# Kernel optimization log

Measured on AMD Instinct MI355X. Metric: run time of the kernel, lower is better.

Reference implementation:

```python
import jax, jax.numpy as jnp
import numpy as np
import math

B, N, D, H = 8, 1024, 512, 8
DH = D // H  # 64
FF = 4 * D   # 2048
SQRT_2_OVER_PI = math.sqrt(2.0 / math.pi)
LN_EPS = 1e-12


def gelu_new(x):
    # tanh-approx GELU as in DenseGatedGeluDense.gelu_new
    return 0.5 * x * (1.0 + jnp.tanh(SQRT_2_OVER_PI * (x + 0.044715 * x ** 3)))


def layer_norm(x, scale, bias):
    m = jnp.mean(x, axis=-1, keepdims=True)
    v = jnp.mean((x - m) ** 2, axis=-1, keepdims=True)
    return (x - m) * jax.lax.rsqrt(v + LN_EPS) * scale + bias


def setup_inputs() -> dict:
    key = jax.random.key(0)
    ks = jax.random.split(key, 12)
    w = lambda k, shape: (jax.random.normal(k, shape, jnp.float32) * 0.02)
    return {
        "X": jax.random.normal(ks[0], (B, N, D), jnp.float32),
        "train_ind": jax.random.randint(ks[1], (B, N), 0, 2).astype(jnp.int32),
        "batch_ind": jax.random.randint(ks[2], (B, N), 0, 2).astype(jnp.int32),
        "Wq": w(ks[3], (D, D)), "bq": jnp.zeros((D,), jnp.float32),
        "Wk": w(ks[4], (D, D)), "bk": jnp.zeros((D,), jnp.float32),
        "Wv": w(ks[5], (D, D)), "bv": jnp.zeros((D,), jnp.float32),
        "Wmix": w(ks[6], (D, D)), "bmix": jnp.zeros((D,), jnp.float32),
        "ln0_s": jnp.ones((D,), jnp.float32), "ln0_b": jnp.zeros((D,), jnp.float32),
        "ln1_s": jnp.ones((D,), jnp.float32), "ln1_b": jnp.zeros((D,), jnp.float32),
        "wi0": w(ks[7], (D, FF)),
        "wi1": w(ks[8], (D, FF)),
        "wo": w(ks[9], (FF, D)),
    }


def reference(X, train_ind, batch_ind, Wq, bq, Wk, bk, Wv, bv, Wmix, bmix,
              ln0_s, ln0_b, ln1_s, ln1_b, wi0, wi1, wo):
    # --- MAB with self-attention (SAB: Y = X), pre-LayerNorm variant ---
    Xn = layer_norm(X, ln0_s, ln0_b)          # ln0 applied to query side only
    Q = Xn @ Wq + bq                           # (B, N, D)
    X_res = Q                                  # fc_res is None -> residual = Q
    K = X @ Wk + bk                            # K/V computed from raw Y (=X)
    V = X @ Wv + bv

    Qh = Q.reshape(B, N, H, DH)
    Kh = K.reshape(B, N, H, DH)
    Vh = V.reshape(B, N, H, DH)

    # scores scaled by sqrt(dim_KV) per att_score_norm == 'softmax'
    scores = jnp.einsum("bqhd,bkhd->bhqk", Qh, Kh) / math.sqrt(D)  # (B,H,N,N)

    # get_attention_mask: key j attendable iff j in train or batch set, or j == i
    allowed_key = (train_ind + batch_ind) != 0                     # (B, N)
    allow = allowed_key[:, None, :] | jnp.eye(N, dtype=bool)[None] # (B, N, N)
    scores = jnp.where(allow[:, None, :, :], scores, -jnp.inf)

    A = jax.nn.softmax(scores, axis=-1)
    O = jnp.einsum("bhqk,bkhd->bqhd", A, Vh).reshape(B, N, D)

    Hc = O @ Wmix + bmix                       # fc_mix_heads
    Hc = X_res + Hc                            # residual (pre-LN branch)

    # GEGLU rFF block (DenseGatedGeluDense), pre-LN
    x1 = layer_norm(Hc, ln1_s, ln1_b)
    ff = (gelu_new(x1 @ wi0) * (x1 @ wi1)) @ wo
    return Hc + ff
```

## Files before the change

### kernel.cpp

```cpp
#include <hip/hip_runtime.h>
#include <hip/hip_bf16.h>
#include <math.h>

#define DEV __device__ __forceinline__

using bf16x8 = __attribute__((ext_vector_type(8))) short;
using f32x4  = __attribute__((ext_vector_type(4))) float;

static constexpr int Bb = 8, Nn = 1024, Dd = 512, Hh = 8, DHd = 64, FFd = 2048;
static constexpr int Mrows = Bb * Nn;

DEV short f2bf(float f) {
  union { float f; unsigned u; } v; v.f = f;
  unsigned r = v.u + 0x7fffu + ((v.u >> 16) & 1u);
  return (short)(r >> 16);
}
DEV float bf2f(short s) {
  union { unsigned u; float f; } v; v.u = ((unsigned)(unsigned short)s) << 16;
  return v.f;
}
DEV float fexp2(float x) { return __builtin_amdgcn_exp2f(x); }

DEV f32x4 mfma16(bf16x8 a, bf16x8 b, f32x4 c) {
  return __builtin_amdgcn_mfma_f32_16x16x32_bf16(a, b, c, 0, 0, 0);
}

DEV size_t swz(int r, int k, int ld) {
  return (size_t)(r >> 6) * 64 * ld + (size_t)(k >> 3) * 512
       + (size_t)((r & 63) * 8 + (k & 7));
}

DEV void gload16(const void* g, void* l) {
  __builtin_amdgcn_global_load_lds(
      (const __attribute__((address_space(1))) void*)g,
      (__attribute__((address_space(3))) void*)l, 16, 0, 0);
}

DEV float gelu_fast(float g) {
  float u2l = 2.30220822f * (g + 0.044715f * g * g * g);
  return g / (1.0f + fexp2(-u2l));
}

DEV void xcd_tile2(int wg, int gx, int gy, int& trow, int& tcol) {
  int xcd = wg & 7, idx = wg >> 3;
  int XC = (gx >= 16) ? 2 : 1, XR = 8 / XC;
  int lcx = gx / XC, lcy = gy / XR;
  trow = (xcd / XC) * lcy + idx / lcx;
  tcol = (xcd % XC) * lcx + idx % lcx;
}

struct PreArgs {
  const float* src[7]; short* dst[7];
  const int* train; const int* batch; char* allowC;
  const float* X; const float* sc; const float* bi;
  short* xn; short* xraw;
};
__global__ __launch_bounds__(256)
void k_preprocess(PreArgs a) {
  __shared__ float tile[32][33];
  int id = blockIdx.x;
  if (id < 4096) {
    int j, rem;
    if (id < 1024)      { j = id >> 8;                 rem = id & 255; }
    else if (id < 3072) { j = 4 + ((id - 1024) >> 10); rem = (id - 1024) & 1023; }
    else                { j = 6;                       rem = id - 3072; }
    int K = (j == 6) ? 2048 : 512;
    int N = (j == 4 || j == 5) ? 2048 : 512;
    const float* W = a.src[j];
    short* WT = a.dst[j];
    int gx = N >> 5;
    int nb = (rem % gx) * 32, kb = (rem / gx) * 32;
    int tx = threadIdx.x & 31, ty = threadIdx.x >> 5;
    #pragma unroll
    for (int i = ty; i < 32; i += 8)
      tile[i][tx] = W[(size_t)(kb + i) * N + nb + tx];
    __syncthreads();
    #pragma unroll
    for (int i = ty; i < 32; i += 8)
      WT[swz(nb + i, kb + tx, K)] = f2bf(tile[tx][i]);
  } else if (id < 4128) {
    int i = (id - 4096) * 256 + threadIdx.x;
    a.allowC[i] = ((a.train[i] | a.batch[i]) != 0) ? 1 : 0;
  } else {
    int w = threadIdx.x >> 6, lane = threadIdx.x & 63;
    int row = (id - 4128) * 4 + w;
    const float* x = a.X + (size_t)row * Dd + lane * 8;
    f32x4 va = *(const f32x4*)x;
    f32x4 vb = *(const f32x4*)(x + 4);
    float p = va[0] + va[1] + va[2] + va[3] + vb[0] + vb[1] + vb[2] + vb[3];
    #pragma unroll
    for (int off = 1; off < 64; off <<= 1) p += __shfl_xor(p, off);
    float mean = p * (1.0f / Dd);
    float d[8];
    #pragma unroll
    for (int j = 0; j < 4; j++) { d[j] = va[j] - mean; d[4 + j] = vb[j] - mean; }
    float q = 0.0f;
    #pragma unroll
    for (int j = 0; j < 8; j++) q += d[j] * d[j];
    #pragma unroll
    for (int off = 1; off < 64; off <<= 1) q += __shfl_xor(q, off);
    float rs = rsqrtf(q * (1.0f / Dd) + 1e-12f);
    int c0 = lane * 8;
    f32x4 s0 = *(const f32x4*)(a.sc + c0), s1 = *(const f32x4*)(a.sc + c0 + 4);
    f32x4 b0 = *(const f32x4*)(a.bi + c0), b1 = *(const f32x4*)(a.bi + c0 + 4);
    bf16x8 o;
    #pragma unroll
    for (int j = 0; j < 4; j++) {
      o[j]     = f2bf(d[j] * rs * s0[j] + b0[j]);
      o[4 + j] = f2bf(d[4 + j] * rs * s1[j] + b1[j]);
    }
    *(bf16x8*)(a.xn + swz(row, c0, Dd)) = o;
    bf16x8 rv;
    #pragma unroll
    for (int j = 0; j < 4; j++) { rv[j] = f2bf(va[j]); rv[4 + j] = f2bf(vb[j]); }
    *(bf16x8*)(a.xraw + swz(row, c0, Dd)) = rv;
  }
}

__global__ __launch_bounds__(256)
void k_layernorm1(const float* __restrict__ X, const float* __restrict__ sc,
                  const float* __restrict__ bi, short* __restrict__ out) {
  int w = threadIdx.x >> 6, lane = threadIdx.x & 63;
  int row = blockIdx.x * 4 + w;
  const float* x = X + (size_t)row * Dd + lane * 8;
  f32x4 a = *(const f32x4*)x;
  f32x4 b = *(const f32x4*)(x + 4);
  float p = a[0] + a[1] + a[2] + a[3] + b[0] + b[1] + b[2] + b[3];
  #pragma unroll
  for (int off = 1; off < 64; off <<= 1) p += __shfl_xor(p, off);
  float mean = p * (1.0f / Dd);
  float d[8];
  #pragma unroll
  for (int j = 0; j < 4; j++) { d[j] = a[j] - mean; d[4 + j] = b[j] - mean; }
  float q = 0.0f;
  #pragma unroll
  for (int j = 0; j < 8; j++) q += d[j] * d[j];
  #pragma unroll
  for (int off = 1; off < 64; off <<= 1) q += __shfl_xor(q, off);
  float rs = rsqrtf(q * (1.0f / Dd) + 1e-12f);
  int c0 = lane * 8;
  f32x4 s0 = *(const f32x4*)(sc + c0), s1 = *(const f32x4*)(sc + c0 + 4);
  f32x4 b0 = *(const f32x4*)(bi + c0), b1 = *(const f32x4*)(bi + c0 + 4);
  bf16x8 o;
  #pragma unroll
  for (int j = 0; j < 4; j++) {
    o[j]     = f2bf(d[j] * rs * s0[j] + b0[j]);
    o[4 + j] = f2bf(d[4 + j] * rs * s1[j] + b1[j]);
  }
  *(bf16x8*)(out + swz(row, c0, Dd)) = o;
}

template<int BN, int BK, int BIASM, int RESM, bool WF, bool WB, int EPI>
__global__ __launch_bounds__(256, 4)
void k_gemm128(const short* __restrict__ A, const short* __restrict__ BT,
               const float* __restrict__ bias, const float* __restrict__ resF,
               const short* __restrict__ resB, const short* __restrict__ gpre,
               float* __restrict__ outF, short* __restrict__ outB,
               int M, int N, int K) {
  constexpr int FN = BN / 32;
  __shared__ short lA[2][128 * BK];
  __shared__ short lB[2][BN * BK];
  int tid = threadIdx.x, w = tid >> 6, lane = tid & 63;
  int lr = lane & 15, lg = lane >> 4;
  int wr = w >> 1, wc = w & 1;
  int trow, tcol;
  xcd_tile2(blockIdx.y * gridDim.x + blockIdx.x, gridDim.x, gridDim.y, trow, tcol);
  int row0 = trow * 128, col0 = tcol * BN;
  f32x4 acc[4][FN] = {};

  auto stage = [&](int buf, int k0) {
    #pragma unroll
    for (int i = 0; i < BK / 16; i++) {
      int c = i * 4 + w;
      gload16(A + swz(row0 + (c & 1) * 64 + lane, k0 + (c >> 1) * 8, K),
              &lA[buf][c * 512]);
    }
    #pragma unroll
    for (int i = 0; i < (BN * BK) / 2048; i++) {
      int c = i * 4 + w;
      if (BN == 128)
        gload16(BT + swz(col0 + (c & 1) * 64 + lane, k0 + (c >> 1) * 8, K),
                &lB[buf][c * 512]);
      else
        gload16(BT + swz(col0 + lane, k0 + c * 8, K), &lB[buf][c * 512]);
    }
  };

  stage(0, 0);
  __syncthreads();
  int nt = K / BK, buf = 0;
  for (int t = 0; t < nt; t++) {
    if (t + 1 < nt) stage(buf ^ 1, (t + 1) * BK);
    #pragma unroll
    for (int kk = 0; kk < BK / 32; kk++) {
      bf16x8 af[4];
      #pragma unroll
      for (int m = 0; m < 4; m++)
        af[m] = *(const bf16x8*)&lA[buf][(kk * 4 + lg) * 1024 + (wr * 64 + m * 16 + lr) * 8];
      #pragma unroll
      for (int n = 0; n < FN; n++) {
        bf16x8 bfr = *(const bf16x8*)&lB[buf][(kk * 4 + lg) * (BN * 8)
                                              + (wc * (BN / 2) + n * 16 + lr) * 8];
        #pragma unroll
        for (int m = 0; m < 4; m++)
          acc[m][n] = mfma16(af[m], bfr, acc[m][n]);
      }
    }
    __syncthreads();
    buf ^= 1;
  }

  #pragma unroll
  for (int n = 0; n < FN; n++) {
    int col = col0 + wc * (BN / 2) + n * 16 + lr;
    float bv = (BIASM == 1) ? bias[col] : 0.0f;
    #pragma unroll
    for (int m = 0; m < 4; m++) {
      #pragma unroll
      for (int r = 0; r < 4; r++) {
        int rowg = row0 + wr * 64 + m * 16 + lg * 4 + r;
        float vv = acc[m][n][r] + bv;
        if (BIASM == 2) vv += bias[rowg];
        if (RESM == 1) vv += resF[(size_t)rowg * N + col];
        if (RESM == 2) vv += bf2f(resB[swz(rowg, col, N)]);
        if (EPI == 1) vv = gelu_fast(vv);
        if (EPI == 2) vv *= bf2f(gpre[swz(rowg, col, N)]);
        if (WF) outF[(size_t)rowg * N + col] = vv;
        if (WB) outB[swz(rowg, col, N)] = f2bf(vv);
      }
    }
  }
}

__global__ __launch_bounds__(256, 4)
void k_qkv(const short* __restrict__ Xnbf, const short* __restrict__ Xbf,
           const short* __restrict__ WqT, const short* __restrict__ WkT,
           const short* __restrict__ WvT,
           const float* __restrict__ bq, const float* __restrict__ bk,
           const float* __restrict__ bv,
           short* __restrict__ Qbf, short* __restrict__ Kbf,
           short* __restrict__ VTg) {
  constexpr int BN = 64, BK = 64, FN = 2;
  constexpr int K = 512;
  __shared__ short lA[2][128 * BK];
  __shared__ short lB[2][BN * BK];
  int id = blockIdx.x;
  int which = id >> 9, sub = id & 511;
  const short *A, *BT; const float* bias; short* outB;
  int N, gx, gy; bool rowbias;
  if (which == 0)      { A = Xnbf; BT = WqT; bias = bq; outB = Qbf; N = 512;  gx = 8;   gy = 64; rowbias = false; }
  else if (which == 1) { A = Xbf;  BT = WkT; bias = bk; outB = Kbf; N = 512;  gx = 8;   gy = 64; rowbias = false; }
  else                 { A = WvT;  BT = Xbf; bias = bv; outB = VTg; N = 8192; gx = 128; gy = 4;  rowbias = true;  }
  int tid = threadIdx.x, w = tid >> 6, lane = tid & 63;
  int lr = lane & 15, lg = lane >> 4;
  int wr = w >> 1, wc = w & 1;
  int trow, tcol;
  xcd_tile2(sub, gx, gy, trow, tcol);
  int row0 = trow * 128, col0 = tcol * BN;
  f32x4 acc[4][FN] = {};

  auto stage = [&](int buf, int k0) {
    #pragma unroll
    for (int i = 0; i < BK / 16; i++) {
      int c = i * 4 + w;
      gload16(A + swz(row0 + (c & 1) * 64 + lane, k0 + (c >> 1) * 8, K),
              &lA[buf][c * 512]);
    }
    #pragma unroll
    for (int i = 0; i < (BN * BK) / 2048; i++) {
      int c = i * 4 + w;
      gload16(BT + swz(col0 + lane, k0 + c * 8, K), &lB[buf][c * 512]);
    }
  };

  stage(0, 0);
  __syncthreads();
  int nt = K / BK, buf = 0;
  for (int t = 0; t < nt; t++) {
    if (t + 1 < nt) stage(buf ^ 1, (t + 1) * BK);
    #pragma unroll
    for (int kk = 0; kk < BK / 32; kk++) {
      bf16x8 af[4];
      #pragma unroll
      for (int m = 0; m < 4; m++)
        af[m] = *(const bf16x8*)&lA[buf][(kk * 4 + lg) * 1024 + (wr * 64 + m * 16 + lr) * 8];
      #pragma unroll
      for (int n = 0; n < FN; n++) {
        bf16x8 bfr = *(const bf16x8*)&lB[buf][(kk * 4 + lg) * (BN * 8)
                                              + (wc * (BN / 2) + n * 16 + lr) * 8];
        #pragma unroll
        for (int m = 0; m < 4; m++)
          acc[m][n] = mfma16(af[m], bfr, acc[m][n]);
      }
    }
    __syncthreads();
    buf ^= 1;
  }

  #pragma unroll
  for (int n = 0; n < FN; n++) {
    int col = col0 + wc * (BN / 2) + n * 16 + lr;
    float bvc = rowbias ? 0.0f : bias[col];
    #pragma unroll
    for (int m = 0; m < 4; m++) {
      #pragma unroll
      for (int r = 0; r < 4; r++) {
        int rowg = row0 + wr * 64 + m * 16 + lg * 4 + r;
        float vv = acc[m][n][r] + bvc;
        if (rowbias) vv += bias[rowg];
        outB[swz(rowg, col, N)] = f2bf(vv);
      }
    }
  }
}

__global__ __launch_bounds__(256, 2)
void k_attention(const short* __restrict__ Qbf, const short* __restrict__ Kbf,
                 const short* __restrict__ VT, const char* __restrict__ allowC,
                 short* __restrict__ Obf) {
  __shared__ __align__(16) short Plds[4][32][72];
  __shared__ float maskF[Nn];
  int bid = blockIdx.x;
  int h = bid & 7, b = (bid >> 3) & 7, qt = bid >> 6;
  int tid = threadIdx.x, w = tid >> 6, lane = tid & 63, lr = lane & 15, lg = lane >> 4;
  int q0 = qt * 128 + w * 32;

  {
    const char* ac = allowC + b * Nn;
    #pragma unroll
    for (int j = 0; j < 4; j++) {
      int i = tid * 4 + j;
      maskF[i] = ac[i] ? 0.0f : -1e30f;
    }
  }
  __syncthreads();

  bf16x8 aq[2][2];
  #pragma unroll
  for (int qi = 0; qi < 2; qi++)
  #pragma unroll
  for (int j = 0; j < 2; j++)
    aq[qi][j] = *(const bf16x8*)(Qbf + swz(b * Nn + q0 + qi * 16 + lr,
                                           h * 64 + j * 32 + lg * 8, Dd));
  f32x4 acco[2][4] = {};
  float m_run[2][4], l_run[2][4];
  #pragma unroll
  for (int qi = 0; qi < 2; qi++)
  #pragma unroll
  for (int r = 0; r < 4; r++) { m_run[qi][r] = 0.0f; l_run[qi][r] = 0.0f; }
  const float scale2 = 0.06375871573f;

  auto loadK = [&](bf16x8 (&kf)[4][2], int kb) {
    #pragma unroll
    for (int sub = 0; sub < 4; sub++)
    #pragma unroll
    for (int j = 0; j < 2; j++)
      kf[sub][j] = *(const bf16x8*)(Kbf + swz(b * Nn + kb + sub * 16 + lr,
                                              h * 64 + j * 32 + lg * 8, Dd));
  };

  auto process = [&](bf16x8 (&kf)[4][2], int kb, bf16x8 (&kfn)[4][2], int kbn) {
    loadK(kfn, kbn);
    bf16x8 vb[2][4];
    #pragma unroll
    for (int ks = 0; ks < 2; ks++)
    #pragma unroll
    for (int t = 0; t < 4; t++)
      vb[ks][t] = *(const bf16x8*)(VT + swz(h * 64 + t * 16 + lr,
                                            b * Nn + kb + ks * 32 + lg * 8, Mrows));
    f32x4 accs[2][4] = {};
    #pragma unroll
    for (int sub = 0; sub < 4; sub++) {
      #pragma unroll
      for (int qi = 0; qi < 2; qi++) {
        accs[qi][sub] = mfma16(aq[qi][0], kf[sub][0], accs[qi][sub]);
        accs[qi][sub] = mfma16(aq[qi][1], kf[sub][1], accs[qi][sub]);
      }
    }
    float mk[4];
    #pragma unroll
    for (int sub = 0; sub < 4; sub++) mk[sub] = maskF[kb + sub * 16 + lr];
    float sv[2][4][4];
    #pragma unroll
    for (int qi = 0; qi < 2; qi++)
    #pragma unroll
    for (int sub = 0; sub < 4; sub++)
    #pragma unroll
    for (int r = 0; r < 4; r++)
      sv[qi][sub][r] = accs[qi][sub][r] * scale2 + mk[sub];
    if (kb == (q0 & ~63)) {
      #pragma unroll
      for (int qi = 0; qi < 2; qi++)
      #pragma unroll
      for (int sub = 0; sub < 4; sub++) {
        int key = kb + sub * 16 + lr;
        #pragma unroll
        for (int r = 0; r < 4; r++) {
          int qrow = q0 + qi * 16 + lg * 4 + r;
          if (key == qrow) sv[qi][sub][r] = accs[qi][sub][r] * scale2;
        }
      }
    }
    bool allok = true;
    float pmax[2][4];
    #pragma unroll
    for (int qi = 0; qi < 2; qi++)
    #pragma unroll
    for (int r = 0; r < 4; r++) {
      pmax[qi][r] = fmaxf(fmaxf(sv[qi][0][r], sv[qi][1][r]),
                          fmaxf(sv[qi][2][r], sv[qi][3][r]));
      allok = allok && (pmax[qi][r] <= m_run[qi][r] + 11.5416f);
    }
    if (!__all(allok)) {
      #pragma unroll
      for (int qi = 0; qi < 2; qi++)
      #pragma unroll
      for (int r = 0; r < 4; r++) {
        float m = pmax[qi][r];
        #pragma unroll
        for (int off = 1; off < 16; off <<= 1) m = fmaxf(m, __shfl_xor(m, off));
        float mtot = fmaxf(m_run[qi][r], m);
        float alpha = fexp2(m_run[qi][r] - mtot);
        l_run[qi][r] *= alpha;
        m_run[qi][r] = mtot;
        #pragma unroll
        for (int t = 0; t < 4; t++) acco[qi][t][r] *= alpha;
      }
    }
    #pragma unroll
    for (int qi = 0; qi < 2; qi++)
    #pragma unroll
    for (int sub = 0; sub < 4; sub++)
    #pragma unroll
    for (int r = 0; r < 4; r++) {
      float e = fexp2(sv[qi][sub][r] - m_run[qi][r]);
      l_run[qi][r] += e;
      Plds[w][qi * 16 + lg * 4 + r][sub * 16 + lr] = f2bf(e);
    }
    #pragma unroll
    for (int ks = 0; ks < 2; ks++) {
      bf16x8 pa0 = *(const bf16x8*)(&Plds[w][lr][ks * 32 + lg * 8]);
      bf16x8 pa1 = *(const bf16x8*)(&Plds[w][16 + lr][ks * 32 + lg * 8]);
      #pragma unroll
      for (int t = 0; t < 4; t++) {
        acco[0][t] = mfma16(pa0, vb[ks][t], acco[0][t]);
        acco[1][t] = mfma16(pa1, vb[ks][t], acco[1][t]);
      }
    }
  };

  bf16x8 kfA[4][2], kfB[4][2];
  loadK(kfA, 0);
  for (int kb = 0; kb < Nn; kb += 128) {
    int n1 = kb + 64;
    int n2 = (kb + 128 < Nn) ? (kb + 128) : 0;
    process(kfA, kb, kfB, n1);
    process(kfB, n1, kfA, n2);
  }

  #pragma unroll
  for (int qi = 0; qi < 2; qi++)
  #pragma unroll
  for (int r = 0; r < 4; r++) {
    float lsum = l_run[qi][r];
    #pragma unroll
    for (int off = 1; off < 16; off <<= 1) lsum += __shfl_xor(lsum, off);
    l_run[qi][r] = lsum;
  }
  #pragma unroll
  for (int qi = 0; qi < 2; qi++)
  #pragma unroll
  for (int t = 0; t < 4; t++)
  #pragma unroll
  for (int r = 0; r < 4; r++) {
    int q = b * Nn + q0 + qi * 16 + lg * 4 + r;
    Obf[swz(q, h * 64 + t * 16 + lr, Dd)] = f2bf(acco[qi][t][r] / l_run[qi][r]);
  }
}

extern "C" void kernel_launch(void* const* d_in, const int* in_sizes, int n_in,
                              void* d_out, int out_size, void* d_ws, size_t ws_size,
                              hipStream_t stream) {
  const float* X    = (const float*)d_in[0];
  const int*   train= (const int*)d_in[1];
  const int*   batch= (const int*)d_in[2];
  const float* Wq   = (const float*)d_in[3];
  const float* bq   = (const float*)d_in[4];
  const float* Wk   = (const float*)d_in[5];
  const float* bk   = (const float*)d_in[6];
  const float* Wv   = (const float*)d_in[7];
  const float* bv   = (const float*)d_in[8];
  const float* Wmix = (const float*)d_in[9];
  const float* bmix = (const float*)d_in[10];
  const float* ln0s = (const float*)d_in[11];
  const float* ln0b = (const float*)d_in[12];
  const float* ln1s = (const float*)d_in[13];
  const float* ln1b = (const float*)d_in[14];
  const float* wi0  = (const float*)d_in[15];
  const float* wi1  = (const float*)d_in[16];
  const float* wo   = (const float*)d_in[17];
  float* out = (float*)d_out;

  char* ws = (char*)d_ws;
  size_t off = 0;
  auto alloc = [&](size_t bytes) {
    off = (off + 255) & ~(size_t)255;
    void* p = ws + off; off += bytes; return p;
  };
  short* Xbf   = (short*)alloc((size_t)Mrows * Dd * 2);
  short* Xnbf  = (short*)alloc((size_t)Mrows * Dd * 2);
  short* Qbf   = (short*)alloc((size_t)Mrows * Dd * 2);
  short* Kbf   = (short*)alloc((size_t)Mrows * Dd * 2);
  short* VTg   = (short*)alloc((size_t)Dd * Mrows * 2);
  short* Obf   = (short*)alloc((size_t)Mrows * Dd * 2);
  short* x1bf  = (short*)alloc((size_t)Mrows * Dd * 2);
  short* Gbf   = (short*)alloc((size_t)Mrows * FFd * 2);
  short* FFbf  = (short*)alloc((size_t)Mrows * FFd * 2);
  short* WqT   = (short*)alloc((size_t)Dd * Dd * 2);
  short* WkT   = (short*)alloc((size_t)Dd * Dd * 2);
  short* WvT   = (short*)alloc((size_t)Dd * Dd * 2);
  short* WmixT = (short*)alloc((size_t)Dd * Dd * 2);
  short* wi0T  = (short*)alloc((size_t)FFd * Dd * 2);
  short* wi1T  = (short*)alloc((size_t)FFd * Dd * 2);
  short* woT   = (short*)alloc((size_t)Dd * FFd * 2);
  float* Hcf   = (float*)alloc((size_t)Mrows * Dd * 4);
  char*  allowC= (char*)alloc((size_t)Mrows);

  dim3 blk(256);
  PreArgs pa;
  pa.src[0] = Wq;   pa.dst[0] = WqT;
  pa.src[1] = Wk;   pa.dst[1] = WkT;
  pa.src[2] = Wv;   pa.dst[2] = WvT;
  pa.src[3] = Wmix; pa.dst[3] = WmixT;
  pa.src[4] = wi0;  pa.dst[4] = wi0T;
  pa.src[5] = wi1;  pa.dst[5] = wi1T;
  pa.src[6] = wo;   pa.dst[6] = woT;
  pa.train = train; pa.batch = batch; pa.allowC = allowC;
  pa.X = X; pa.sc = ln0s; pa.bi = ln0b; pa.xn = Xnbf; pa.xraw = Xbf;
  k_preprocess<<<6176, blk, 0, stream>>>(pa);

  k_qkv<<<1536, blk, 0, stream>>>(Xnbf, Xbf, WqT, WkT, WvT, bq, bk, bv,
                                  Qbf, Kbf, VTg);

  k_attention<<<Bb * Hh * (Nn / 128), blk, 0, stream>>>(Qbf, Kbf, VTg, allowC, Obf);

  k_gemm128<64, 64, 1, 2, true, false, 0><<<dim3(Dd / 64, Mrows / 128), blk, 0, stream>>>(
      Obf, WmixT, bmix, nullptr, Qbf, nullptr, Hcf, nullptr, Mrows, Dd, Dd);

  k_layernorm1<<<Mrows / 4, blk, 0, stream>>>(Hcf, ln1s, ln1b, x1bf);

  k_gemm128<128, 32, 0, 0, false, true, 1><<<dim3(FFd / 128, Mrows / 128), blk, 0, stream>>>(
      x1bf, wi0T, nullptr, nullptr, nullptr, nullptr, nullptr, Gbf, Mrows, FFd, Dd);
  k_gemm128<128, 32, 0, 0, false, true, 2><<<dim3(FFd / 128, Mrows / 128), blk, 0, stream>>>(
      x1bf, wi1T, nullptr, nullptr, nullptr, Gbf, nullptr, FFbf, Mrows, FFd, Dd);

  k_gemm128<64, 64, 0, 1, true, false, 0><<<dim3(Dd / 64, Mrows / 128), blk, 0, stream>>>(
      FFbf, woT, nullptr, Hcf, nullptr, nullptr, out, nullptr, Mrows, Dd, FFd);
}
```

Baseline: 189.2 us.

## Fuse GEGLU gate and up projections into one dual-accumulator GEMM kernel

Replaces the two separate wi0/wi1 GEMMs, which wrote the GELU result to an intermediate bf16 buffer and read it back, with a single kernel that computes both products for the same A tile and applies gelu(a0)*a1 in the epilogue. This drops the 32 MB round trip through the Gbf buffer, one launch, and the second read of x1. The tile width shrinks to 64 columns with two accumulator sets, so the kernel uses more registers and LDS per block, which may lower occupancy.

Result: faster. 172.7 us (-8.7%).

```diff
diff --git a/kernel.cpp b/kernel.cpp
--- a/kernel.cpp
+++ b/kernel.cpp
@@ -150,11 +150,11 @@
   *(bf16x8*)(out + swz(row, c0, Dd)) = o;
 }
 
-template<int BN, int BK, int BIASM, int RESM, bool WF, bool WB, int EPI>
+template<int BN, int BK, int BIASM, int RESM, bool WF, bool WB>
 __global__ __launch_bounds__(256, 4)
 void k_gemm128(const short* __restrict__ A, const short* __restrict__ BT,
                const float* __restrict__ bias, const float* __restrict__ resF,
-               const short* __restrict__ resB, const short* __restrict__ gpre,
+               const short* __restrict__ resB,
                float* __restrict__ outF, short* __restrict__ outB,
                int M, int N, int K) {
   constexpr int FN = BN / 32;
@@ -223,10 +223,75 @@
         if (BIASM == 2) vv += bias[rowg];
         if (RESM == 1) vv += resF[(size_t)rowg * N + col];
         if (RESM == 2) vv += bf2f(resB[swz(rowg, col, N)]);
-        if (EPI == 1) vv = gelu_fast(vv);
-        if (EPI == 2) vv *= bf2f(gpre[swz(rowg, col, N)]);
         if (WF) outF[(size_t)rowg * N + col] = vv;
         if (WB) outB[swz(rowg, col, N)] = f2bf(vv);
+      }
+    }
+  }
+}
+
+__global__ __launch_bounds__(256, 4)
+void k_geglu64(const short* __restrict__ A, const short* __restrict__ BT0,
+               const short* __restrict__ BT1, short* __restrict__ outB) {
+  constexpr int BN = 64, BK = 32, K = 512, N = 2048;
+  __shared__ short lA[2][128 * BK];
+  __shared__ short lB0[2][BN * BK];
+  __shared__ short lB1[2][BN * BK];
+  int tid = threadIdx.x, w = tid >> 6, lane = tid & 63;
+  int lr = lane & 15, lg = lane >> 4;
+  int wr = w >> 1, wc = w & 1;
+  int trow, tcol;
+  xcd_tile2(blockIdx.x, N / BN, Mrows / 128, trow, tcol);
+  int row0 = trow * 128, col0 = tcol * BN;
+  f32x4 acc0[4][2] = {}, acc1[4][2] = {};
+
+  auto stage = [&](int buf, int k0) {
+    #pragma unroll
+    for (int i = 0; i < 2; i++) {
+      int c = i * 4 + w;
+      gload16(A + swz(row0 + (c & 1) * 64 + lane, k0 + (c >> 1) * 8, K),
+              &lA[buf][c * 512]);
+    }
+    {
+      int c = w;
+      gload16(BT0 + swz(col0 + lane, k0 + c * 8, K), &lB0[buf][c * 512]);
+      gload16(BT1 + swz(col0 + lane, k0 + c * 8, K), &lB1[buf][c * 512]);
+    }
+  };
+
+  stage(0, 0);
+  __syncthreads();
+  int nt = K / BK, buf = 0;
+  for (int t = 0; t < nt; t++) {
+    if (t + 1 < nt) stage(buf ^ 1, (t + 1) * BK);
+    bf16x8 af[4];
+    #pragma unroll
+    for (int m = 0; m < 4; m++)
+      af[m] = *(const bf16x8*)&lA[buf][lg * 1024 + (wr * 64 + m * 16 + lr) * 8];
+    #pragma unroll
+    for (int n = 0; n < 2; n++) {
+      bf16x8 b0 = *(const bf16x8*)&lB0[buf][lg * (BN * 8) + (wc * 32 + n * 16 + lr) * 8];
+      #pragma unroll
+      for (int m = 0; m < 4; m++)
+        acc0[m][n] = mfma16(af[m], b0, acc0[m][n]);
+      bf16x8 b1 = *(const bf16x8*)&lB1[buf][lg * (BN * 8) + (wc * 32 + n * 16 + lr) * 8];
+      #pragma unroll
+      for (int m = 0; m < 4; m++)
+        acc1[m][n] = mfma16(af[m], b1, acc1[m][n]);
+    }
+    __syncthreads();
+    buf ^= 1;
+  }
+
+  #pragma unroll
+  for (int n = 0; n < 2; n++) {
+    int col = col0 + wc * 32 + n * 16 + lr;
+    #pragma unroll
+    for (int m = 0; m < 4; m++) {
+      #pragma unroll
+      for (int r = 0; r < 4; r++) {
+        int rowg = row0 + wr * 64 + m * 16 + lg * 4 + r;
+        outB[swz(rowg, col, N)] = f2bf(gelu_fast(acc0[m][n][r]) * acc1[m][n][r]);
       }
     }
   }
@@ -514,7 +579,6 @@
   short* VTg   = (short*)alloc((size_t)Dd * Mrows * 2);
   short* Obf   = (short*)alloc((size_t)Mrows * Dd * 2);
   short* x1bf  = (short*)alloc((size_t)Mrows * Dd * 2);
-  short* Gbf   = (short*)alloc((size_t)Mrows * FFd * 2);
   short* FFbf  = (short*)alloc((size_t)Mrows * FFd * 2);
   short* WqT   = (short*)alloc((size_t)Dd * Dd * 2);
   short* WkT   = (short*)alloc((size_t)Dd * Dd * 2);
@@ -544,16 +608,13 @@
 
   k_attention<<<Bb * Hh * (Nn / 128), blk, 0, stream>>>(Qbf, Kbf, VTg, allowC, Obf);
 
-  k_gemm128<64, 64, 1, 2, true, false, 0><<<dim3(Dd / 64, Mrows / 128), blk, 0, stream>>>(
-      Obf, WmixT, bmix, nullptr, Qbf, nullptr, Hcf, nullptr, Mrows, Dd, Dd);
+  k_gemm128<64, 64, 1, 2, true, false><<<dim3(Dd / 64, Mrows / 128), blk, 0, stream>>>(
+      Obf, WmixT, bmix, nullptr, Qbf, Hcf, nullptr, Mrows, Dd, Dd);
 
   k_layernorm1<<<Mrows / 4, blk, 0, stream>>>(Hcf, ln1s, ln1b, x1bf);
 
-  k_gemm128<128, 32, 0, 0, false, true, 1><<<dim3(FFd / 128, Mrows / 128), blk, 0, stream>>>(
-      x1bf, wi0T, nullptr, nullptr, nullptr, nullptr, nullptr, Gbf, Mrows, FFd, Dd);
-  k_gemm128<128, 32, 0, 0, false, true, 2><<<dim3(FFd / 128, Mrows / 128), blk, 0, stream>>>(
-      x1bf, wi1T, nullptr, nullptr, nullptr, Gbf, nullptr, FFbf, Mrows, FFd, Dd);
-
-  k_gemm128<64, 64, 0, 1, true, false, 0><<<dim3(Dd / 64, Mrows / 128), blk, 0, stream>>>(
-      FFbf, woT, nullptr, Hcf, nullptr, nullptr, out, nullptr, Mrows, Dd, FFd);
-}
+  k_geglu64<<<2048, blk, 0, stream>>>(x1bf, wi0T, wi1T, FFbf);
+
+  k_gemm128<64, 64, 0, 1, true, false><<<dim3(Dd / 64, Mrows / 128), blk, 0, stream>>>(
+      FFbf, woT, nullptr, Hcf, nullptr, out, nullptr, Mrows, Dd, FFd);
+}
```
